# Optimization experiments

Measured on AMD Instinct MI355X. Metric: run time of the kernel, lower is better.

Reference implementation:

```python
import jax, jax.numpy as jnp
import numpy as np

D1, D2, B, I, O = 64, 64, 32, 64, 128


def setup_inputs() -> dict:
    key = jax.random.key(0)
    ks = jax.random.split(key, 13)
    k = float(np.sqrt(1.0 / O))
    u = lambda kk, shape: jax.random.uniform(kk, shape, minval=-k, maxval=k, dtype=jnp.float32)
    return {
        "x": jax.random.normal(ks[0], (D1, D2, B, I), dtype=jnp.float32),
        "wf": u(ks[1], (2, I, O)),
        "uf": u(ks[2], (2, 2, O)),
        "biasf": u(ks[3], (2, O)),
        "wi": u(ks[4], (I, O)),
        "ui": u(ks[5], (2, O)),
        "biasi": u(ks[6], (O,)),
        "wo": u(ks[7], (I, O)),
        "uo": u(ks[8], (2, O)),
        "biaso": u(ks[9], (O,)),
        "wc": u(ks[10], (I, O)),
        "uc": u(ks[11], (2, O)),
        "biasc": u(ks[12], (O,)),
    }


def reference(x, wf, uf, biasf, wi, ui, biasi, wo, uo, biaso, wc, uc, biasc):
    # x: (D1, D2, B, I). Recurrence: cell (i,j) depends on (i-1,j) [k=0] and (i,j-1) [k=1].
    d1, d2, b, _ = x.shape
    o_dim = wi.shape[1]

    def cell(xj, s0, h0):
        # s0, h0: (2, B, O); index 0 = up-neighbor (dim 0), 1 = left-neighbor (dim 1)
        f = jax.nn.sigmoid(biasf[:, None, :]
                           + jnp.einsum('bi,lio->lbo', xj, wf)
                           + jnp.einsum('kbo,lko->lbo', h0, uf))
        i = jax.nn.sigmoid(biasi + xj @ wi + (h0 * ui[:, None, :]).sum(0))
        og = jax.nn.sigmoid(biaso + xj @ wo + (h0 * uo[:, None, :]).sum(0))
        c = jax.nn.sigmoid(biasc + xj @ wc + (h0 * uc[:, None, :]).sum(0))  # note: sigmoid, as in source
        s = i * c + (f * s0).sum(0)
        h = og * jnp.tanh(s)
        return s, h

    z_row = jnp.zeros((d2, b, o_dim), x.dtype)
    z = jnp.zeros((b, o_dim), x.dtype)

    def row_step(carry, x_row):
        s_up_row, h_up_row = carry  # (D2, B, O) each: previous row's states

        def col_step(c2, inp):
            s_left, h_left = c2
            xj, s_up, h_up = inp
            s, h = cell(xj, jnp.stack([s_up, s_left]), jnp.stack([h_up, h_left]))
            return (s, h), (s, h)

        _, (s_row, h_row) = jax.lax.scan(col_step, (z, z), (x_row, s_up_row, h_up_row))
        return (s_row, h_row), s_row

    _, s_all = jax.lax.scan(row_step, (z_row, z_row), x)
    # Original module returns reshape(s, ...) (cell state), not h -- reproduce faithfully.
    return s_all  # (D1, D2, B, O)
```

## Files before the change

kernel.cpp:

```cpp
#include <hip/hip_runtime.h>
#include <hip/hip_fp16.h>


#define P23_OFF  ((size_t)64 << 20)
#define P4_OFF   ((size_t)128 << 20)
#define GX_BYTES ((size_t)160 << 20)
#define LOG2E    1.4426950408889634f

typedef __attribute__((ext_vector_type(8))) _Float16 half8;
typedef __attribute__((ext_vector_type(2))) __fp16 fp16x2;
typedef __attribute__((ext_vector_type(4))) float f32x4;
typedef __attribute__((ext_vector_type(2))) float f32x2;

__device__ __forceinline__ unsigned pkrtz(float a, float b) {
    union { fp16x2 h; unsigned u; } c;
    c.h = __builtin_amdgcn_cvt_pkrtz(a, b);
    return c.u;
}

__device__ __forceinline__ int diag_off(int d) {
    return (d < 64) ? ((d * (d + 1)) >> 1) : (4096 - (((127 - d) * (128 - d)) >> 1));
}

__global__ __launch_bounds__(256) void lut_kernel(int* __restrict__ lut) {
    int t = blockIdx.x * 256 + threadIdx.x;
    int i = t >> 6, j = t & 63;
    int d = i + j;
    int jmin = (d > 63) ? (d - 63) : 0;
    lut[diag_off(d) + j - jmin] = t;
}

__global__ __launch_bounds__(256) void prep_w(
    const float* __restrict__ wf, const float* __restrict__ wi,
    const float* __restrict__ wo, const float* __restrict__ wc,
    _Float16* __restrict__ wt)
{
    const int g = blockIdx.x;
    const float* W = (g == 0) ? wf : (g == 1) ? (wf + 8192)
                   : (g == 2) ? wi : (g == 3) ? wo : wc;
    const int t = threadIdx.x;
    const int o = t >> 1, k0 = (t & 1) * 32;
    _Float16 buf[32];
#pragma unroll
    for (int k = 0; k < 32; ++k)
        buf[k] = (_Float16)(-W[(k0 + k) * 128 + o] * LOG2E);
    _Float16* dst = wt + ((size_t)g * 128 + o) * 64 + k0;
#pragma unroll
    for (int q = 0; q < 4; ++q) *(half8*)(dst + q * 8) = *(half8*)(buf + q * 8);
}

__global__ __launch_bounds__(256, 4) void gemm_kernel(
    const float* __restrict__ x, const _Float16* __restrict__ wt,
    const float* __restrict__ biasf, const float* __restrict__ biasi,
    const float* __restrict__ biaso, const float* __restrict__ biasc,
    const int* __restrict__ lut, char* __restrict__ gx)
{
    __shared__ _Float16 As[128][72];
    const int t  = threadIdx.x;
    const int p0 = blockIdx.x * 128;
    const int b  = blockIdx.y;

    {
        int r = t >> 1, k0 = (t & 1) * 32;
        int cell = lut[p0 + r];
        const float* xr = x + ((size_t)cell * 32 + b) * 64 + k0;
#pragma unroll
        for (int it = 0; it < 4; ++it) {
            float4 v0 = *(const float4*)(xr + it * 8);
            float4 v1 = *(const float4*)(xr + it * 8 + 4);
            half8 h;
            h[0] = (_Float16)v0.x; h[1] = (_Float16)v0.y;
            h[2] = (_Float16)v0.z; h[3] = (_Float16)v0.w;
            h[4] = (_Float16)v1.x; h[5] = (_Float16)v1.y;
            h[6] = (_Float16)v1.z; h[7] = (_Float16)v1.w;
            *(half8*)&As[r][k0 + it * 8] = h;
        }
    }
    __syncthreads();

    const int lane = t & 63;
    const int wv   = __builtin_amdgcn_readfirstlane(t >> 6);
    const int m    = lane & 15;
    const int quad = lane >> 4;
    const int o0   = wv * 32 + m;
    const int o1   = o0 + 16;
    const size_t row0 = (size_t)(b * 128 + o0) * 4096;
    const size_t row1 = (size_t)(b * 128 + o1) * 4096;
    const int pq = p0 + quad * 4;

    auto pair_phase = [&](const _Float16* wga, const _Float16* wgb,
                          const float* bA, const float* bB, char* plane) {
        half8 ba0[2], ba1[2], bb0[2], bb1[2];
#pragma unroll
        for (int kh = 0; kh < 2; ++kh) {
            ba0[kh] = *(const half8*)(wga + o0 * 64 + kh * 32 + quad * 8);
            ba1[kh] = *(const half8*)(wga + o1 * 64 + kh * 32 + quad * 8);
            bb0[kh] = *(const half8*)(wgb + o0 * 64 + kh * 32 + quad * 8);
            bb1[kh] = *(const half8*)(wgb + o1 * 64 + kh * 32 + quad * 8);
        }
        float sA0 = -bA[o0] * LOG2E, sA1 = -bA[o1] * LOG2E;
        float sB0 = -bB[o0] * LOG2E, sB1 = -bB[o1] * LOG2E;
#pragma unroll
        for (int pf = 0; pf < 8; ++pf) {
            half8 af0 = *(const half8*)&As[pf * 16 + m][quad * 8];
            half8 af1 = *(const half8*)&As[pf * 16 + m][32 + quad * 8];
            f32x4 aA0 = {}, aA1 = {}, aB0 = {}, aB1 = {};
            aA0 = __builtin_amdgcn_mfma_f32_16x16x32_f16(af0, ba0[0], aA0, 0, 0, 0);
            aA0 = __builtin_amdgcn_mfma_f32_16x16x32_f16(af1, ba0[1], aA0, 0, 0, 0);
            aA1 = __builtin_amdgcn_mfma_f32_16x16x32_f16(af0, ba1[0], aA1, 0, 0, 0);
            aA1 = __builtin_amdgcn_mfma_f32_16x16x32_f16(af1, ba1[1], aA1, 0, 0, 0);
            aB0 = __builtin_amdgcn_mfma_f32_16x16x32_f16(af0, bb0[0], aB0, 0, 0, 0);
            aB0 = __builtin_amdgcn_mfma_f32_16x16x32_f16(af1, bb0[1], aB0, 0, 0, 0);
            aB1 = __builtin_amdgcn_mfma_f32_16x16x32_f16(af0, bb1[0], aB1, 0, 0, 0);
            aB1 = __builtin_amdgcn_mfma_f32_16x16x32_f16(af1, bb1[1], aB1, 0, 0, 0);
            uint4 st0, st1;
            st0.x = pkrtz(aA0[0] + sA0, aB0[0] + sB0);
            st0.y = pkrtz(aA0[1] + sA0, aB0[1] + sB0);
            st0.z = pkrtz(aA0[2] + sA0, aB0[2] + sB0);
            st0.w = pkrtz(aA0[3] + sA0, aB0[3] + sB0);
            *(uint4*)(plane + (row0 + pq + pf * 16) * 4) = st0;
            st1.x = pkrtz(aA1[0] + sA1, aB1[0] + sB1);
            st1.y = pkrtz(aA1[1] + sA1, aB1[1] + sB1);
            st1.z = pkrtz(aA1[2] + sA1, aB1[2] + sB1);
            st1.w = pkrtz(aA1[3] + sA1, aB1[3] + sB1);
            *(uint4*)(plane + (row1 + pq + pf * 16) * 4) = st1;
        }
    };
    pair_phase(wt,            wt + 8192,     biasf, biasf + 128, gx);
    pair_phase(wt + 2 * 8192, wt + 3 * 8192, biasi, biaso,       gx + P23_OFF);

    {
        const _Float16* wg = wt + 4 * 8192;
        half8 b0[2], b1[2];
#pragma unroll
        for (int kh = 0; kh < 2; ++kh) {
            b0[kh] = *(const half8*)(wg + o0 * 64 + kh * 32 + quad * 8);
            b1[kh] = *(const half8*)(wg + o1 * 64 + kh * 32 + quad * 8);
        }
        float s0 = -biasc[o0] * LOG2E, s1 = -biasc[o1] * LOG2E;
        char* plane = gx + P4_OFF;
#pragma unroll
        for (int pf = 0; pf < 8; ++pf) {
            half8 af0 = *(const half8*)&As[pf * 16 + m][quad * 8];
            half8 af1 = *(const half8*)&As[pf * 16 + m][32 + quad * 8];
            f32x4 ac0 = {}, ac1 = {};
            ac0 = __builtin_amdgcn_mfma_f32_16x16x32_f16(af0, b0[0], ac0, 0, 0, 0);
            ac0 = __builtin_amdgcn_mfma_f32_16x16x32_f16(af1, b0[1], ac0, 0, 0, 0);
            ac1 = __builtin_amdgcn_mfma_f32_16x16x32_f16(af0, b1[0], ac1, 0, 0, 0);
            ac1 = __builtin_amdgcn_mfma_f32_16x16x32_f16(af1, b1[1], ac1, 0, 0, 0);
            uint2 st0, st1;
            st0.x = pkrtz(ac0[0] + s0, ac0[1] + s0);
            st0.y = pkrtz(ac0[2] + s0, ac0[3] + s0);
            *(uint2*)(plane + (row0 + pq + pf * 16) * 2) = st0;
            st1.x = pkrtz(ac1[0] + s1, ac1[1] + s1);
            st1.y = pkrtz(ac1[2] + s1, ac1[3] + s1);
            *(uint2*)(plane + (row1 + pq + pf * 16) * 2) = st1;
        }
    }
}

__global__ __launch_bounds__(256) void recur_kernel(
    char* __restrict__ gx,
    const float* __restrict__ uf, const float* __restrict__ ui,
    const float* __restrict__ uo, const float* __restrict__ uc)
{
    const int lane = threadIdx.x & 63;
    const int w = __builtin_amdgcn_readfirstlane(blockIdx.x * 4 + (threadIdx.x >> 6));
    const int o = w & 127;

    const f32x2 nAu = { -uf[o]       * LOG2E, -uf[256 + o] * LOG2E };
    const f32x2 nAl = { -uf[128 + o] * LOG2E, -uf[384 + o] * LOG2E };
    const f32x2 nBu = { -ui[o]       * LOG2E, -uo[o]       * LOG2E };
    const f32x2 nBl = { -ui[128 + o] * LOG2E, -uo[128 + o] * LOG2E };
    const float nc0 = -uc[o] * LOG2E, nc1 = -uc[128 + o] * LOG2E;

    const char* pc01 = gx + (size_t)w * 16384;
    const char* pc23 = gx + P23_OFF + (size_t)w * 16384;
    const char* pc4  = gx + P4_OFF + (size_t)w * 8192;
    char*       ps4  = gx + P4_OFF + (size_t)w * 8192;
    const int l4 = lane * 4, l2 = lane * 2;

    const int zm  = (lane == 0) ? 0 : -1;
    const int bpi = (lane - 1) * 4;

    f32x2 c01, c23, n01, n23;
    float c4, n4;

#define LD3(v01_, v23_, v4_) { \
    __half2 h01 = *(const __half2*)(pc01 + l4); \
    __half2 h23 = *(const __half2*)(pc23 + l4); \
    _Float16 h4 = *(const _Float16*)(pc4 + l2); \
    v01_ = (f32x2){ __low2float(h01), __high2float(h01) }; \
    v23_ = (f32x2){ __low2float(h23), __high2float(h23) }; \
    v4_ = (float)h4; }

    LD3(c01, c23, c4); pc01 += 4;  pc23 += 4;  pc4 += 2;
    LD3(n01, n23, n4); pc01 += 8;  pc23 += 8;  pc4 += 4;

    float s_prev = 0.f, h_prev = 0.f;

#pragma unroll 2
    for (int d = 0; d < 127; ++d) {
        f32x2 t01, t23; float t4;
        LD3(t01, t23, t4);
        int del = min(d + 3, 124 - d); del = max(del, 0);
        pc01 += del * 4; pc23 += del * 4; pc4 += del * 2;

        int slb = __builtin_amdgcn_ds_bpermute(bpi, __float_as_int(s_prev)) & zm;
        int hlb = __builtin_amdgcn_ds_bpermute(bpi, __float_as_int(h_prev)) & zm;
        float sl = __int_as_float(slb), hl = __int_as_float(hlb);

        f32x2 hu2 = { h_prev, h_prev };
        f32x2 hl2 = { hl, hl };
        f32x2 zA = __builtin_elementwise_fma(hu2, nAu,
                     __builtin_elementwise_fma(hl2, nAl, c01));
        f32x2 zB = __builtin_elementwise_fma(hu2, nBu,
                     __builtin_elementwise_fma(hl2, nBl, c23));
        float zc = fmaf(h_prev, nc0, fmaf(hl, nc1, c4));

        f32x2 eA = { __builtin_amdgcn_exp2f(zA.x), __builtin_amdgcn_exp2f(zA.y) };
        f32x2 eB = { __builtin_amdgcn_exp2f(zB.x), __builtin_amdgcn_exp2f(zB.y) };
        float ec = __builtin_amdgcn_exp2f(zc);
        f32x2 aA = eA + 1.f;
        f32x2 aB = eB + 1.f;
        float acg = ec + 1.f;

        float mff  = aA.x * aA.y;
        float mic  = aB.x * acg;
        float den  = mff * mic;
        float num  = fmaf(s_prev, aA.y, sl * aA.x);
        float num2 = fmaf(num, mic, mff);
        float s    = num2 * __builtin_amdgcn_rcpf(den);

        float t2 = fminf(s * (2.f * LOG2E), 80.f);
        float e2 = __builtin_amdgcn_exp2f(t2);
        float hd = fmaf(aB.y, e2, aB.y);
        float h  = (e2 - 1.f) * __builtin_amdgcn_rcpf(hd);

        bool act = (unsigned)(d - lane) < 64u;
        if (act) *(_Float16*)(ps4 + l2) = (_Float16)s;
        ps4 += min(d + 1, 126 - d) * 2;

        s_prev = act ? s : 0.f;
        h_prev = act ? h : 0.f;
        c01 = n01; c23 = n23; c4 = n4;
        n01 = t01; n23 = t23; n4 = t4;
    }
#undef LD3
}

__global__ __launch_bounds__(256) void transpose_kernel(
    const char* __restrict__ gx, const int* __restrict__ lut,
    float* __restrict__ out)
{
    __shared__ _Float16 T[256][80];
    const _Float16* p4 = (const _Float16*)(gx + P4_OFF);
    const int t  = threadIdx.x;
    const int p0 = blockIdx.x * 64;
    const int w0 = blockIdx.y * 256;
#pragma unroll
    for (int it = 0; it < 8; ++it) {
        int wl = it * 32 + (t >> 3), pl = (t & 7) * 8;
        *(half8*)&T[wl][pl] =
            *(const half8*)(p4 + (size_t)(w0 + wl) * 4096 + p0 + pl);
    }
    __syncthreads();
    float* ob = out + w0 + t;
#pragma unroll 4
    for (int p = 0; p < 64; ++p) {
        int cell = lut[p0 + p];
        ob[(size_t)cell * 4096] = (float)T[t][p];
    }
}

extern "C" void kernel_launch(void* const* d_in, const int* in_sizes, int n_in,
                              void* d_out, int out_size, void* d_ws, size_t ws_size,
                              hipStream_t stream) {
    const float* x     = (const float*)d_in[0];
    const float* wf    = (const float*)d_in[1];
    const float* uf    = (const float*)d_in[2];
    const float* biasf = (const float*)d_in[3];
    const float* wi    = (const float*)d_in[4];
    const float* ui    = (const float*)d_in[5];
    const float* biasi = (const float*)d_in[6];
    const float* wo    = (const float*)d_in[7];
    const float* uo    = (const float*)d_in[8];
    const float* biaso = (const float*)d_in[9];
    const float* wc    = (const float*)d_in[10];
    const float* uc    = (const float*)d_in[11];
    const float* biasc = (const float*)d_in[12];
    float* out = (float*)d_out;

    char*     gx  = (char*)d_ws;
    int*      lut = (int*)(gx + GX_BYTES);
    _Float16* wt  = (_Float16*)((char*)lut + 16384);

    lut_kernel<<<16, 256, 0, stream>>>(lut);
    prep_w<<<5, 256, 0, stream>>>(wf, wi, wo, wc, wt);
    gemm_kernel<<<dim3(32, 32), 256, 0, stream>>>(
        x, wt, biasf, biasi, biaso, biasc, lut, gx);
    recur_kernel<<<1024, 256, 0, stream>>>(gx, uf, ui, uo, uc);
    transpose_kernel<<<dim3(64, 16), 256, 0, stream>>>(gx, lut, out);
}
```

Baseline: 240.8 us.

## Tile gate-preactivation buffer by 128-cell diagonal tiles for contiguous GEMM stores

Changes the workspace layout of the precomputed gate preactivations from per-(batch,output) rows of 4096 cells to tiles of 128 diagonal-ordered cells, each tile holding all (batch,output) rows contiguously. GEMM stores from a block now land in one contiguous region instead of being strided 16 KB apart. The recurrence and transpose kernels compute tile-based offsets per step, which adds some address arithmetic. The recurrence's per-wave loads also become more scattered across tiles.

```diff
diff --git a/kernel.cpp b/kernel.cpp
--- a/kernel.cpp
+++ b/kernel.cpp
@@ -57,7 +57,8 @@
 {
     __shared__ _Float16 As[128][72];
     const int t  = threadIdx.x;
-    const int p0 = blockIdx.x * 128;
+    const int pt = blockIdx.x;
+    const int p0 = pt * 128;
     const int b  = blockIdx.y;
 
     {
@@ -84,9 +85,9 @@
     const int quad = lane >> 4;
     const int o0   = wv * 32 + m;
     const int o1   = o0 + 16;
-    const size_t row0 = (size_t)(b * 128 + o0) * 4096;
-    const size_t row1 = (size_t)(b * 128 + o1) * 4096;
-    const int pq = p0 + quad * 4;
+
+    const size_t t01 = (size_t)pt * 2097152 + (size_t)(b * 128) * 512;
+    const size_t t4b = (size_t)pt * 1048576 + (size_t)(b * 128) * 256;
 
     auto pair_phase = [&](const _Float16* wga, const _Float16* wgb,
                           const float* bA, const float* bB, char* plane) {
@@ -100,6 +101,7 @@
         }
         float sA0 = -bA[o0] * LOG2E, sA1 = -bA[o1] * LOG2E;
         float sB0 = -bB[o0] * LOG2E, sB1 = -bB[o1] * LOG2E;
+        char* base = plane + t01;
 #pragma unroll
         for (int pf = 0; pf < 8; ++pf) {
             half8 af0 = *(const half8*)&As[pf * 16 + m][quad * 8];
@@ -118,12 +120,12 @@
             st0.y = pkrtz(aA0[1] + sA0, aB0[1] + sB0);
             st0.z = pkrtz(aA0[2] + sA0, aB0[2] + sB0);
             st0.w = pkrtz(aA0[3] + sA0, aB0[3] + sB0);
-            *(uint4*)(plane + (row0 + pq + pf * 16) * 4) = st0;
+            *(uint4*)(base + (size_t)o0 * 512 + quad * 16 + pf * 64) = st0;
             st1.x = pkrtz(aA1[0] + sA1, aB1[0] + sB1);
             st1.y = pkrtz(aA1[1] + sA1, aB1[1] + sB1);
             st1.z = pkrtz(aA1[2] + sA1, aB1[2] + sB1);
             st1.w = pkrtz(aA1[3] + sA1, aB1[3] + sB1);
-            *(uint4*)(plane + (row1 + pq + pf * 16) * 4) = st1;
+            *(uint4*)(base + (size_t)o1 * 512 + quad * 16 + pf * 64) = st1;
         }
     };
     pair_phase(wt,            wt + 8192,     biasf, biasf + 128, gx);
@@ -138,7 +140,7 @@
             b1[kh] = *(const half8*)(wg + o1 * 64 + kh * 32 + quad * 8);
         }
         float s0 = -biasc[o0] * LOG2E, s1 = -biasc[o1] * LOG2E;
-        char* plane = gx + P4_OFF;
+        char* base = gx + P4_OFF + t4b;
 #pragma unroll
         for (int pf = 0; pf < 8; ++pf) {
             half8 af0 = *(const half8*)&As[pf * 16 + m][quad * 8];
@@ -151,10 +153,10 @@
             uint2 st0, st1;
             st0.x = pkrtz(ac0[0] + s0, ac0[1] + s0);
             st0.y = pkrtz(ac0[2] + s0, ac0[3] + s0);
-            *(uint2*)(plane + (row0 + pq + pf * 16) * 2) = st0;
+            *(uint2*)(base + (size_t)o0 * 256 + quad * 8 + pf * 32) = st0;
             st1.x = pkrtz(ac1[0] + s1, ac1[1] + s1);
             st1.y = pkrtz(ac1[2] + s1, ac1[3] + s1);
-            *(uint2*)(plane + (row1 + pq + pf * 16) * 2) = st1;
+            *(uint2*)(base + (size_t)o1 * 256 + quad * 8 + pf * 32) = st1;
         }
     }
 }
@@ -174,37 +176,45 @@
     const f32x2 nBl = { -ui[128 + o] * LOG2E, -uo[128 + o] * LOG2E };
     const float nc0 = -uc[o] * LOG2E, nc1 = -uc[128 + o] * LOG2E;
 
-    const char* pc01 = gx + (size_t)w * 16384;
-    const char* pc23 = gx + P23_OFF + (size_t)w * 16384;
-    const char* pc4  = gx + P4_OFF + (size_t)w * 8192;
-    char*       ps4  = gx + P4_OFF + (size_t)w * 8192;
-    const int l4 = lane * 4, l2 = lane * 2;
+    const char* b01 = gx + (size_t)w * 512;
+    const char* b23 = gx + P23_OFF + (size_t)w * 512;
+    const char* b4  = gx + P4_OFF + (size_t)w * 256;
+    char*       s4  = gx + P4_OFF + (size_t)w * 256;
 
     const int zm  = (lane == 0) ? 0 : -1;
     const int bpi = (lane - 1) * 4;
 
+    auto offs = [&](int pb) -> int {
+        int p = pb + lane;
+        return ((p >> 7) << 21) + ((p & 127) << 2);
+    };
+
     f32x2 c01, c23, n01, n23;
     float c4, n4;
 
-#define LD3(v01_, v23_, v4_) { \
-    __half2 h01 = *(const __half2*)(pc01 + l4); \
-    __half2 h23 = *(const __half2*)(pc23 + l4); \
-    _Float16 h4 = *(const _Float16*)(pc4 + l2); \
+#define LD3(off_, v01_, v23_, v4_) { \
+    __half2 h01 = *(const __half2*)(b01 + (off_)); \
+    __half2 h23 = *(const __half2*)(b23 + (off_)); \
+    _Float16 h4 = *(const _Float16*)(b4 + ((off_) >> 1)); \
     v01_ = (f32x2){ __low2float(h01), __high2float(h01) }; \
     v23_ = (f32x2){ __low2float(h23), __high2float(h23) }; \
     v4_ = (float)h4; }
 
-    LD3(c01, c23, c4); pc01 += 4;  pc23 += 4;  pc4 += 2;
-    LD3(n01, n23, n4); pc01 += 8;  pc23 += 8;  pc4 += 4;
+    int offA = offs(0);
+    int offB = offs(1);
+    LD3(offA, c01, c23, c4);
+    LD3(offB, n01, n23, n4);
+    int pb = 3;
 
     float s_prev = 0.f, h_prev = 0.f;
 
 #pragma unroll 2
     for (int d = 0; d < 127; ++d) {
+        int offC = offs(pb);
         f32x2 t01, t23; float t4;
-        LD3(t01, t23, t4);
+        LD3(offC, t01, t23, t4);
         int del = min(d + 3, 124 - d); del = max(del, 0);
-        pc01 += del * 4; pc23 += del * 4; pc4 += del * 2;
+        pb += del;
 
         int slb = __builtin_amdgcn_ds_bpermute(bpi, __float_as_int(s_prev)) & zm;
         int hlb = __builtin_amdgcn_ds_bpermute(bpi, __float_as_int(h_prev)) & zm;
@@ -238,13 +248,13 @@
         float h  = (e2 - 1.f) * __builtin_amdgcn_rcpf(hd);
 
         bool act = (unsigned)(d - lane) < 64u;
-        if (act) *(_Float16*)(ps4 + l2) = (_Float16)s;
-        ps4 += min(d + 1, 126 - d) * 2;
+        if (act) *(_Float16*)(s4 + (offA >> 1)) = (_Float16)s;
 
         s_prev = act ? s : 0.f;
         h_prev = act ? h : 0.f;
         c01 = n01; c23 = n23; c4 = n4;
         n01 = t01; n23 = t23; n4 = t4;
+        offA = offB; offB = offC;
     }
 #undef LD3
 }
@@ -254,15 +264,17 @@
     float* __restrict__ out)
 {
     __shared__ _Float16 T[256][80];
-    const _Float16* p4 = (const _Float16*)(gx + P4_OFF);
     const int t  = threadIdx.x;
     const int p0 = blockIdx.x * 64;
     const int w0 = blockIdx.y * 256;
+    const int pt  = p0 >> 7;
+    const int pl0 = p0 & 127;
+    const char* p4t = gx + P4_OFF + (size_t)pt * 1048576;
 #pragma unroll
     for (int it = 0; it < 8; ++it) {
         int wl = it * 32 + (t >> 3), pl = (t & 7) * 8;
         *(half8*)&T[wl][pl] =
-            *(const half8*)(p4 + (size_t)(w0 + wl) * 4096 + p0 + pl);
+            *(const half8*)(p4t + (size_t)(w0 + wl) * 256 + (pl0 + pl) * 2);
     }
     __syncthreads();
     float* ob = out + w0 + t;
```

After: 229.9 us. 1.05x faster.
